# Kernel tuning notes

Hardware: AMD Instinct MI355X
Metric: run time of the kernel (lower is better)

## Reference

```python
import jax, jax.numpy as jnp
import numpy as np

# ---- model constants (match init_kwargs) ----
B, N, T, L = 16384, 32, 300, 1
DIM = 2                      # len(state_index)
DT = 1.0 / (T * L)           # dt = 1/(T*l)
STEPS = T * L                # Euler integration steps (time_steps = STEPS+1)
A_X = 1.0                    # canonical DMP phase constant
TAU = 1.0
HID = 64
OUT = N * DIM + DIM          # fc2_mean output size


def setup_inputs() -> dict:
    key = jax.random.key(0)
    ks = jax.random.split(key, 8)
    s = lambda i, shape, scale: jax.random.normal(ks[i], shape, jnp.float32) * scale
    inp = {
        "state": jax.random.normal(ks[0], (B, 3), jnp.float32),
        "fc1_w": s(1, (HID, 3), 0.3),
        "fc1_b": jnp.full((HID,), 0.1, jnp.float32),
        "fc2m_w": s(2, (OUT, HID), 0.1),
        "fc2m_b": jnp.full((OUT,), 0.1, jnp.float32),
        "sig_w": s(3, (DIM, HID), 0.1),
        "sig_b": jnp.zeros((DIM,), jnp.float32),
        "val_w": s(4, (DIM, HID), 0.1),
        "val_b": jnp.zeros((DIM,), jnp.float32),
    }
    # DMPParameters: gaussian RBF centers on exp-decayed phase, canonical widths
    c = jnp.exp(-A_X * jnp.linspace(0.0, 1.0, N))
    inp["dmp_c"] = c.astype(jnp.float32)
    inp["dmp_sigma2"] = (N ** 1.5 / c / A_X).astype(jnp.float32)
    return inp


def dmp_rollout(w, goal, y0, dy0, a_z, c, sigma2):
    """Euler rollout of DMP transformation system.
    w: [M,N] basis weights, goal/y0/dy0/a_z: [M] per-channel scalars.
    Returns Y, dY, ddY each [M, STEPS+1]."""
    z0 = dy0 * TAU
    b_z = a_z / 4.0

    def step(carry, _):
        x, y, z = carry
        x = x + (-A_X * x) * TAU * DT                       # phase update
        psi = jnp.exp(-0.5 * (x - c) ** 2 / sigma2)          # [N] gaussian RBF
        fx = (w @ psi) * x * (goal - y0) / jnp.sum(psi)      # [M] forcing term
        dz = a_z * (b_z * (goal - y) - z) + fx
        dy = z
        y = y + TAU * dy * DT
        z = z + TAU * dz * DT
        return (x, y, z), (y, dy * TAU, dz * TAU)

    _, (Ys, dYs, ddYs) = jax.lax.scan(
        step, (jnp.float32(1.0), y0, z0), None, length=STEPS)
    Y = jnp.concatenate([y0[None], Ys], axis=0).T            # [M, STEPS+1]
    dY = jnp.concatenate([dy0[None], dYs], axis=0).T
    ddY = jnp.concatenate([z0[None], ddYs], axis=0).T
    return Y, dY, ddY


def reference(state, fc1_w, fc1_b, fc2m_w, fc2m_b, sig_w, sig_b,
              val_w, val_b, dmp_c, dmp_sigma2):
    x = jnp.tanh(state @ fc1_w.T + fc1_b) * 0.1              # [B,64]
    y0 = state[:, :DIM].reshape(-1)                           # [M=B*DIM]
    dy0 = jnp.zeros_like(y0) + 0.01

    # value = fc2_value(x).repeat(1,T).view(-1,T,2).transpose(1,2) == broadcast over T
    v = x @ val_w.T + val_b                                   # [B,2]
    value = jnp.broadcast_to(v[:, :, None], (B, DIM, T))

    sigma = (jax.nn.sigmoid(x @ sig_w.T + sig_b) * 1.0 + 0.001).reshape(-1, DIM, 1)

    ndp_wg = x @ fc2m_w.T + fc2m_b                            # [B, 2N+2]
    goal = ndp_wg[:, :DIM].reshape(-1)                        # [M]
    w = ndp_wg[:, DIM:DIM * (N + 1)].reshape(-1, N)           # [M,N]
    a_z = jnp.clip(ndp_wg[:, -1], 0.5, 30.0)                  # learned a_z (az=True)
    a_z = jnp.broadcast_to(a_z[:, None], (B, DIM)).reshape(-1)

    Y, _, _ = dmp_rollout(w, goal, y0, dy0, a_z, dmp_c, dmp_sigma2)
    y = Y.reshape(B, DIM, -1)[:, :, ::L]                      # [B,2,T+1]
    a = y[:, :, 1:] - y[:, :, :-1]                            # [B,2,T]
    return (a, sigma, value)
```

## Files before the change

kernel.cpp:

```cpp
#include <hip/hip_runtime.h>
#include <hip/hip_bf16.h>

#define NB 32
#define TS 300
#define TSP 304
#define NBATCH 16384
#define DTF (1.0f/300.0f)
#define A_ELEMS (NBATCH*2*TS)

typedef __attribute__((ext_vector_type(8))) short bf16x8;
typedef __attribute__((ext_vector_type(4))) float f32x4;

static __device__ __forceinline__ ushort f2bf(float f) {
    union { __hip_bfloat16 h; ushort u; } cv;
    cv.h = __float2bfloat16(f);
    return cv.u;
}
static __device__ __forceinline__ float rdlane(float v, int lane) {
    return __int_as_float(__builtin_amdgcn_readlane(__float_as_int(v), lane));
}

__global__ __launch_bounds__(256) void k_head(
    const float* __restrict__ state,
    const float* __restrict__ fc1_w, const float* __restrict__ fc1_b,
    const float* __restrict__ fc2m_w, const float* __restrict__ fc2m_b,
    const float* __restrict__ sig_w, const float* __restrict__ sig_b,
    const float* __restrict__ val_w, const float* __restrict__ val_b,
    const float* __restrict__ dmp_c, const float* __restrict__ dmp_s2,
    float* __restrict__ sig_out, float* __restrict__ pbuf,
    ushort* __restrict__ wbuf16, ushort* __restrict__ phiB)
{
    if (blockIdx.x == 512) {
        const float l2 = log2f(1.0f - DTF);
        for (int t = threadIdx.x; t < TSP; t += 256) {
            ushort row[NB];
            if (t < TS) {
                const float x = exp2f((float)(t + 1) * l2);
                float ps[NB]; float s = 0.0f;
                #pragma unroll
                for (int n = 0; n < NB; ++n) {
                    float d = x - dmp_c[n];
                    float p = __expf(-0.5f * d * d / dmp_s2[n]);
                    ps[n] = p; s += p;
                }
                const float inv = x / s;
                #pragma unroll
                for (int n = 0; n < NB; ++n) row[n] = f2bf(ps[n] * inv);
            } else {
                #pragma unroll
                for (int n = 0; n < NB; ++n) row[n] = 0;
            }
            uint4* dst = (uint4*)(phiB + t*NB);
            #pragma unroll
            for (int q4 = 0; q4 < 4; ++q4) {
                union { ushort us[8]; uint4 v; } pk;
                #pragma unroll
                for (int e = 0; e < 8; ++e) pk.us[e] = row[q4*8 + e];
                dst[q4] = pk.v;
            }
        }
        return;
    }

    __shared__ float wlds[70*64];
    __shared__ float f1[64*4];
    const int tid = threadIdx.x;
    const int wv_ = tid >> 6;
    const int j   = tid & 63;

    for (int i = tid; i < 70*64; i += 256) {
        const int row = i >> 6, col = i & 63;
        float v;
        if (row < 66)      v = fc2m_w[i];
        else if (row < 68) v = sig_w[(row-66)*64 + col];
        else               v = val_w[(row-68)*64 + col];
        const int q = col >> 2, e = col & 3;
        wlds[row*64 + (((q ^ (row & 15)) << 2) | e)] = v;
    }
    if (tid < 64) {
        f1[tid*4+0] = fc1_w[tid*3+0];
        f1[tid*4+1] = fc1_w[tid*3+1];
        f1[tid*4+2] = fc1_w[tid*3+2];
        f1[tid*4+3] = fc1_b[tid];
    }
    __syncthreads();

    const int r2 = 64 + (j % 6);
    float wr[64], w2[64];
    #pragma unroll
    for (int q = 0; q < 16; ++q) {
        float4 a  = *(const float4*)(wlds + j*64  + ((q ^ (j  & 15)) << 2));
        wr[q*4+0]=a.x; wr[q*4+1]=a.y; wr[q*4+2]=a.z; wr[q*4+3]=a.w;
        float4 b4 = *(const float4*)(wlds + r2*64 + ((q ^ (r2 & 15)) << 2));
        w2[q*4+0]=b4.x; w2[q*4+1]=b4.y; w2[q*4+2]=b4.z; w2[q*4+3]=b4.w;
    }
    const float bias1 = fc2m_b[j];
    const float bias2 = (r2 < 66) ? fc2m_b[r2] : (r2 < 68) ? sig_b[r2-66] : val_b[r2-68];
    const float4 fw = *(const float4*)(f1 + j*4);

    const int bbase = (blockIdx.x << 5) + (wv_ << 3);
    float sreg = (j < 24) ? state[bbase*3 + j] : 0.0f;

    for (int it = 0; it < 8; ++it) {
        const int b = bbase + it;
        const float s0  = rdlane(sreg, it*3+0);
        const float s1  = rdlane(sreg, it*3+1);
        const float s2v = rdlane(sreg, it*3+2);
        float pre = fmaf(fw.x, s0, fmaf(fw.y, s1, fmaf(fw.z, s2v, fw.w)));
        float e = __expf(2.0f * pre);
        float h = (1.0f - 2.0f/(e + 1.0f)) * 0.1f;
        float a1 = bias1, a1b = 0.0f, a2 = bias2, a2b = 0.0f;
        #pragma unroll
        for (int k = 0; k < 64; k += 2) {
            const float h0 = rdlane(h, k);
            const float h1 = rdlane(h, k+1);
            a1  = fmaf(wr[k],   h0, a1 );
            a1b = fmaf(wr[k+1], h1, a1b);
            a2  = fmaf(w2[k],   h0, a2 );
            a2b = fmaf(w2[k+1], h1, a2b);
        }
        a1 += a1b; a2 += a2b;
        float az = rdlane(a2, 1);
        az = fminf(fmaxf(az, 0.5f), 30.0f);
        const float vv0 = rdlane(a2, 4);
        const float vv1 = rdlane(a2, 5);
        if (j >= 2) wbuf16[b*64 + j - 2]  = f2bf(a1);
        else        wbuf16[b*64 + 62 + j] = f2bf(a2);
        if (j == 2 || j == 3)
            sig_out[b*2 + j - 2] = 1.0f / (1.0f + __expf(-a2)) + 0.001f;
        if (j < 2) {
            const float y0 = (j == 0) ? s0 : s1;
            const float vvl = (j == 0) ? vv0 : vv1;
            *(float4*)(pbuf + (b*2 + j)*4) = make_float4(a1, a1 - y0, az, vvl);
        }
    }
}

__global__ __launch_bounds__(256) void k_rollout(
    const ushort* __restrict__ phiB, const float* __restrict__ pbuf,
    const ushort* __restrict__ wbuf16, float* __restrict__ a_out,
    float* __restrict__ v_out)
{
    __shared__ float tile[256][20];
    const int tid = threadIdx.x;
    const int wv = tid >> 6;
    const int l  = tid & 63;
    const int ch = l & 15;
    const int g  = l >> 4;
    const int m  = (blockIdx.x << 6) + (wv << 4) + ch;

    const float4 pp = *(const float4*)(pbuf + m*4);
    const float az = pp.z;
    const float Ac = DTF * az * az * 0.25f;
    const float Bc = DTF * az;
    const float Kc = DTF * pp.y;
    const float c0 = (g == 0) ? Ac * pp.x : 0.0f;
    float y = (g == 0) ? (pp.x - pp.y) : 0.0f;
    float z = (g == 0) ? 0.01f : 0.0f;

    const bf16x8 wb = *(const bf16x8*)(wbuf16 + m*NB + g*8);
    const bf16x8* ap = (const bf16x8*)(phiB + ch*NB + g*8);
    bf16x8 af = ap[0];

    const float fv = pp.w;
    const f32x4 zacc = {0.0f, 0.0f, 0.0f, 0.0f};
    float4* myrow = (float4*)&tile[tid][0];

    for (int c = 0; c < 19; ++c) {
        f32x4 facc = __builtin_amdgcn_mfma_f32_16x16x32_bf16(af, wb, zacc, 0, 0, 0);
        if (c < 18) af = ap[(c + 1) * 64];
        float av[16];
        #pragma unroll
        for (int i = 0; i < 16; ++i) {
            float f = (g == (i >> 2)) ? facc[i & 3] : 0.0f;
            av[i] = z * DTF;
            float u = z + c0;
            u = fmaf(Kc, f, u);
            u = fmaf(-Bc, z, u);
            z = fmaf(-Ac, y, u);
            y += av[i];
        }
        #pragma unroll
        for (int q = 0; q < 4; ++q)
            myrow[q] = make_float4(av[q*4+0], av[q*4+1], av[q*4+2], av[q*4+3]);

        if (c < 18 || g < 3) {
            float4 s4 = make_float4(0.f, 0.f, 0.f, 0.f);
            #pragma unroll
            for (int gg = 0; gg < 4; ++gg) {
                const float4 v4 = *(const float4*)&tile[(wv << 6) + (gg << 4) + ch][g << 2];
                s4.x += v4.x; s4.y += v4.y; s4.z += v4.z; s4.w += v4.w;
            }
            const int ob = m * TS + c*16 + (g << 2);
            *(float4*)(a_out + ob) = s4;
            *(float4*)(v_out + ob) = make_float4(fv, fv, fv, fv);
        }
    }
}

extern "C" void kernel_launch(void* const* d_in, const int* in_sizes, int n_in,
                              void* d_out, int out_size, void* d_ws, size_t ws_size,
                              hipStream_t stream) {
    (void)in_sizes; (void)n_in; (void)out_size; (void)ws_size;
    const float* state  = (const float*)d_in[0];
    const float* fc1_w  = (const float*)d_in[1];
    const float* fc1_b  = (const float*)d_in[2];
    const float* fc2m_w = (const float*)d_in[3];
    const float* fc2m_b = (const float*)d_in[4];
    const float* sig_w  = (const float*)d_in[5];
    const float* sig_b  = (const float*)d_in[6];
    const float* val_w  = (const float*)d_in[7];
    const float* val_b  = (const float*)d_in[8];
    const float* dmp_c  = (const float*)d_in[9];
    const float* dmp_s2 = (const float*)d_in[10];

    float* out     = (float*)d_out;
    float* a_out   = out;
    float* sig_out = out + A_ELEMS;
    float* v_out   = out + A_ELEMS + NBATCH*2;

    float* ws     = (float*)d_ws;
    ushort* phiB  = (ushort*)ws;
    float* pbuf   = ws + 8192;
    ushort* wbuf16 = (ushort*)(ws + 8192 + 131072);

    k_head<<<dim3(513), dim3(256), 0, stream>>>(state, fc1_w, fc1_b, fc2m_w, fc2m_b,
                                                sig_w, sig_b, val_w, val_b,
                                                dmp_c, dmp_s2,
                                                sig_out, pbuf, wbuf16, phiB);
    k_rollout<<<dim3(512), dim3(256), 0, stream>>>(phiB, pbuf, wbuf16, a_out, v_out);
}
```

Before: 33.95 us.

## Fuse head and rollout kernels, keep intermediates in LDS, broadcast forcing via permlane

```diff
diff --git a/kernel.cpp b/kernel.cpp
--- a/kernel.cpp
+++ b/kernel.cpp
@@ -3,7 +3,6 @@
 
 #define NB 32
 #define TS 300
-#define TSP 304
 #define NBATCH 16384
 #define DTF (1.0f/300.0f)
 #define A_ELEMS (NBATCH*2*TS)
@@ -20,52 +19,25 @@
     return __int_as_float(__builtin_amdgcn_readlane(__float_as_int(v), lane));
 }
 
-__global__ __launch_bounds__(256) void k_head(
+__global__ __launch_bounds__(256) void k_fused(
     const float* __restrict__ state,
     const float* __restrict__ fc1_w, const float* __restrict__ fc1_b,
     const float* __restrict__ fc2m_w, const float* __restrict__ fc2m_b,
     const float* __restrict__ sig_w, const float* __restrict__ sig_b,
     const float* __restrict__ val_w, const float* __restrict__ val_b,
     const float* __restrict__ dmp_c, const float* __restrict__ dmp_s2,
-    float* __restrict__ sig_out, float* __restrict__ pbuf,
-    ushort* __restrict__ wbuf16, ushort* __restrict__ phiB)
+    float* __restrict__ sig_out, float* __restrict__ a_out,
+    float* __restrict__ v_out)
 {
-    if (blockIdx.x == 512) {
-        const float l2 = log2f(1.0f - DTF);
-        for (int t = threadIdx.x; t < TSP; t += 256) {
-            ushort row[NB];
-            if (t < TS) {
-                const float x = exp2f((float)(t + 1) * l2);
-                float ps[NB]; float s = 0.0f;
-                #pragma unroll
-                for (int n = 0; n < NB; ++n) {
-                    float d = x - dmp_c[n];
-                    float p = __expf(-0.5f * d * d / dmp_s2[n]);
-                    ps[n] = p; s += p;
-                }
-                const float inv = x / s;
-                #pragma unroll
-                for (int n = 0; n < NB; ++n) row[n] = f2bf(ps[n] * inv);
-            } else {
-                #pragma unroll
-                for (int n = 0; n < NB; ++n) row[n] = 0;
-            }
-            uint4* dst = (uint4*)(phiB + t*NB);
-            #pragma unroll
-            for (int q4 = 0; q4 < 4; ++q4) {
-                union { ushort us[8]; uint4 v; } pk;
-                #pragma unroll
-                for (int e = 0; e < 8; ++e) pk.us[e] = row[q4*8 + e];
-                dst[q4] = pk.v;
-            }
-        }
-        return;
-    }
-
-    __shared__ float wlds[70*64];
-    __shared__ float f1[64*4];
+    __shared__ ushort phis[304*NB];
+    __shared__ float  wlds[70*64];
+    __shared__ float  f1[64*4];
+    __shared__ ushort wloc[64*NB];
+    __shared__ float4 ppl[64];
+    __shared__ float4 xt[4][16][5];
+
     const int tid = threadIdx.x;
-    const int wv_ = tid >> 6;
+    const int wv  = tid >> 6;
     const int j   = tid & 63;
 
     for (int i = tid; i < 70*64; i += 256) {
@@ -83,125 +55,159 @@
         f1[tid*4+2] = fc1_w[tid*3+2];
         f1[tid*4+3] = fc1_b[tid];
     }
+    {
+        const float l2 = log2f(1.0f - DTF);
+        for (int t = tid; t < 304; t += 256) {
+            ushort row[NB];
+            if (t < TS) {
+                const float x = exp2f((float)(t + 1) * l2);
+                float ps[NB]; float s = 0.0f;
+                #pragma unroll
+                for (int n = 0; n < NB; ++n) {
+                    float d = x - dmp_c[n];
+                    float p = __expf(-0.5f * d * d / dmp_s2[n]);
+                    ps[n] = p; s += p;
+                }
+                const float inv = x / s;
+                #pragma unroll
+                for (int n = 0; n < NB; ++n) row[n] = f2bf(ps[n] * inv);
+            } else {
+                #pragma unroll
+                for (int n = 0; n < NB; ++n) row[n] = 0;
+            }
+            uint4* dst = (uint4*)(phis + t*NB);
+            #pragma unroll
+            for (int q4 = 0; q4 < 4; ++q4) {
+                union { ushort us[8]; uint4 v; } pk;
+                #pragma unroll
+                for (int e = 0; e < 8; ++e) pk.us[e] = row[q4*8 + e];
+                dst[q4 ^ (t & 3)] = pk.v;
+            }
+        }
+    }
     __syncthreads();
 
-    const int r2 = 64 + (j % 6);
-    float wr[64], w2[64];
-    #pragma unroll
-    for (int q = 0; q < 16; ++q) {
-        float4 a  = *(const float4*)(wlds + j*64  + ((q ^ (j  & 15)) << 2));
-        wr[q*4+0]=a.x; wr[q*4+1]=a.y; wr[q*4+2]=a.z; wr[q*4+3]=a.w;
-        float4 b4 = *(const float4*)(wlds + r2*64 + ((q ^ (r2 & 15)) << 2));
-        w2[q*4+0]=b4.x; w2[q*4+1]=b4.y; w2[q*4+2]=b4.z; w2[q*4+3]=b4.w;
-    }
-    const float bias1 = fc2m_b[j];
-    const float bias2 = (r2 < 66) ? fc2m_b[r2] : (r2 < 68) ? sig_b[r2-66] : val_b[r2-68];
-    const float4 fw = *(const float4*)(f1 + j*4);
-
-    const int bbase = (blockIdx.x << 5) + (wv_ << 3);
-    float sreg = (j < 24) ? state[bbase*3 + j] : 0.0f;
-
-    for (int it = 0; it < 8; ++it) {
-        const int b = bbase + it;
-        const float s0  = rdlane(sreg, it*3+0);
-        const float s1  = rdlane(sreg, it*3+1);
-        const float s2v = rdlane(sreg, it*3+2);
-        float pre = fmaf(fw.x, s0, fmaf(fw.y, s1, fmaf(fw.z, s2v, fw.w)));
-        float e = __expf(2.0f * pre);
-        float h = (1.0f - 2.0f/(e + 1.0f)) * 0.1f;
-        float a1 = bias1, a1b = 0.0f, a2 = bias2, a2b = 0.0f;
+    {
+        const int r2 = 64 + (j % 6);
+        float wr[64], w2[64];
         #pragma unroll
-        for (int k = 0; k < 64; k += 2) {
-            const float h0 = rdlane(h, k);
-            const float h1 = rdlane(h, k+1);
-            a1  = fmaf(wr[k],   h0, a1 );
-            a1b = fmaf(wr[k+1], h1, a1b);
-            a2  = fmaf(w2[k],   h0, a2 );
-            a2b = fmaf(w2[k+1], h1, a2b);
-        }
-        a1 += a1b; a2 += a2b;
-        float az = rdlane(a2, 1);
-        az = fminf(fmaxf(az, 0.5f), 30.0f);
-        const float vv0 = rdlane(a2, 4);
-        const float vv1 = rdlane(a2, 5);
-        if (j >= 2) wbuf16[b*64 + j - 2]  = f2bf(a1);
-        else        wbuf16[b*64 + 62 + j] = f2bf(a2);
-        if (j == 2 || j == 3)
-            sig_out[b*2 + j - 2] = 1.0f / (1.0f + __expf(-a2)) + 0.001f;
-        if (j < 2) {
-            const float y0 = (j == 0) ? s0 : s1;
-            const float vvl = (j == 0) ? vv0 : vv1;
-            *(float4*)(pbuf + (b*2 + j)*4) = make_float4(a1, a1 - y0, az, vvl);
-        }
-    }
-}
-
-__global__ __launch_bounds__(256) void k_rollout(
-    const ushort* __restrict__ phiB, const float* __restrict__ pbuf,
-    const ushort* __restrict__ wbuf16, float* __restrict__ a_out,
-    float* __restrict__ v_out)
-{
-    __shared__ float tile[256][20];
-    const int tid = threadIdx.x;
-    const int wv = tid >> 6;
-    const int l  = tid & 63;
-    const int ch = l & 15;
-    const int g  = l >> 4;
-    const int m  = (blockIdx.x << 6) + (wv << 4) + ch;
-
-    const float4 pp = *(const float4*)(pbuf + m*4);
+        for (int q = 0; q < 16; ++q) {
+            float4 a  = *(const float4*)(wlds + j*64  + ((q ^ (j  & 15)) << 2));
+            wr[q*4+0]=a.x; wr[q*4+1]=a.y; wr[q*4+2]=a.z; wr[q*4+3]=a.w;
+            float4 b4 = *(const float4*)(wlds + r2*64 + ((q ^ (r2 & 15)) << 2));
+            w2[q*4+0]=b4.x; w2[q*4+1]=b4.y; w2[q*4+2]=b4.z; w2[q*4+3]=b4.w;
+        }
+        const float bias1 = fc2m_b[j];
+        const float bias2 = (r2 < 66) ? fc2m_b[r2] : (r2 < 68) ? sig_b[r2-66] : val_b[r2-68];
+        const float4 fw = *(const float4*)(f1 + j*4);
+
+        const int bbase = (blockIdx.x << 5) + (wv << 3);
+        float sreg = (j < 24) ? state[bbase*3 + j] : 0.0f;
+
+        for (int it = 0; it < 8; ++it) {
+            const float s0  = rdlane(sreg, it*3+0);
+            const float s1  = rdlane(sreg, it*3+1);
+            const float s2v = rdlane(sreg, it*3+2);
+            float pre = fmaf(fw.x, s0, fmaf(fw.y, s1, fmaf(fw.z, s2v, fw.w)));
+            float e = __expf(2.0f * pre);
+            float h = (1.0f - 2.0f/(e + 1.0f)) * 0.1f;
+            float a1 = bias1, a1b = 0.0f, a2 = bias2, a2b = 0.0f;
+            #pragma unroll
+            for (int k = 0; k < 64; k += 2) {
+                const float h0 = rdlane(h, k);
+                const float h1 = rdlane(h, k+1);
+                a1  = fmaf(wr[k],   h0, a1 );
+                a1b = fmaf(wr[k+1], h1, a1b);
+                a2  = fmaf(w2[k],   h0, a2 );
+                a2b = fmaf(w2[k+1], h1, a2b);
+            }
+            a1 += a1b; a2 += a2b;
+            float az = rdlane(a2, 1);
+            az = fminf(fmaxf(az, 0.5f), 30.0f);
+            const float vv0 = rdlane(a2, 4);
+            const float vv1 = rdlane(a2, 5);
+            const int chp = (wv << 4) + (it << 1);
+            if (j >= 2) wloc[(chp + ((j-2) >> 5))*NB + ((j-2) & 31)] = f2bf(a1);
+            else        wloc[(chp + 1)*NB + 30 + j]                  = f2bf(a2);
+            if (j == 2 || j == 3)
+                sig_out[(bbase + it)*2 + j - 2] = 1.0f / (1.0f + __expf(-a2)) + 0.001f;
+            if (j < 2) {
+                const float y0 = (j == 0) ? s0 : s1;
+                const float vvl = (j == 0) ? vv0 : vv1;
+                ppl[chp + j] = make_float4(a1, a1 - y0, az, vvl);
+            }
+        }
+    }
+    __syncthreads();
+
+    const int ch = j & 15;
+    const int g  = j >> 4;
+    const int chl = (wv << 4) + ch;
+
+    const float4 pp = ppl[chl];
     const float az = pp.z;
     const float Ac = DTF * az * az * 0.25f;
     const float Bc = DTF * az;
     const float Kc = DTF * pp.y;
-    const float c0 = (g == 0) ? Ac * pp.x : 0.0f;
-    float y = (g == 0) ? (pp.x - pp.y) : 0.0f;
-    float z = (g == 0) ? 0.01f : 0.0f;
-
-    const bf16x8 wb = *(const bf16x8*)(wbuf16 + m*NB + g*8);
-    const bf16x8* ap = (const bf16x8*)(phiB + ch*NB + g*8);
-    bf16x8 af = ap[0];
-
-    const float fv = pp.w;
+    const float c0 = Ac * pp.x;
+    float y = pp.x - pp.y;
+    float z = 0.01f;
+
+    const bf16x8 wb = *(const bf16x8*)(wloc + chl*NB + g*8);
+    const ushort* aprow = phis + ch*NB + ((g ^ (ch & 3)) << 3);
+    bf16x8 af = *(const bf16x8*)aprow;
+
+    const int mloc = j >> 2;
+    const int m_st = (blockIdx.x << 6) + (wv << 4) + mloc;
+    const float fv = ppl[(wv << 4) + mloc].w;
+    const float4 vsp = make_float4(fv, fv, fv, fv);
+    float* aptr = a_out + m_st*TS + (j & 3)*4;
+    float* vptr = v_out + m_st*TS + (j & 3)*4;
+    const bool tail_ok = (j & 3) < 3;
+
     const f32x4 zacc = {0.0f, 0.0f, 0.0f, 0.0f};
-    float4* myrow = (float4*)&tile[tid][0];
 
     for (int c = 0; c < 19; ++c) {
         f32x4 facc = __builtin_amdgcn_mfma_f32_16x16x32_bf16(af, wb, zacc, 0, 0, 0);
-        if (c < 18) af = ap[(c + 1) * 64];
-        float av[16];
+        if (c < 18) af = *(const bf16x8*)(aprow + (c + 1)*16*NB);
+
+        float F[16];
+        #pragma unroll
+        for (int q = 0; q < 4; ++q) {
+            float a = facc[q], b = facc[q];
+            asm volatile("v_permlane16_swap_b32 %0, %1" : "+v"(a), "+v"(b));
+            float a2 = a, b2 = b;
+            asm volatile("v_permlane32_swap_b32 %0, %1" : "+v"(a), "+v"(a2));
+            asm volatile("v_permlane32_swap_b32 %0, %1" : "+v"(b), "+v"(b2));
+            F[0*4+q] = a; F[1*4+q] = b; F[2*4+q] = a2; F[3*4+q] = b2;
+        }
+
+        float avq[4] = {0.f, 0.f, 0.f, 0.f};
         #pragma unroll
         for (int i = 0; i < 16; ++i) {
-            float f = (g == (i >> 2)) ? facc[i & 3] : 0.0f;
-            av[i] = z * DTF;
+            const float aval = z * DTF;
+            if (g == (i >> 2)) avq[i & 3] = aval;
             float u = z + c0;
-            u = fmaf(Kc, f, u);
+            u = fmaf(Kc, F[i], u);
             u = fmaf(-Bc, z, u);
             z = fmaf(-Ac, y, u);
-            y += av[i];
-        }
-        #pragma unroll
-        for (int q = 0; q < 4; ++q)
-            myrow[q] = make_float4(av[q*4+0], av[q*4+1], av[q*4+2], av[q*4+3]);
-
-        if (c < 18 || g < 3) {
-            float4 s4 = make_float4(0.f, 0.f, 0.f, 0.f);
-            #pragma unroll
-            for (int gg = 0; gg < 4; ++gg) {
-                const float4 v4 = *(const float4*)&tile[(wv << 6) + (gg << 4) + ch][g << 2];
-                s4.x += v4.x; s4.y += v4.y; s4.z += v4.z; s4.w += v4.w;
-            }
-            const int ob = m * TS + c*16 + (g << 2);
-            *(float4*)(a_out + ob) = s4;
-            *(float4*)(v_out + ob) = make_float4(fv, fv, fv, fv);
-        }
+            y += aval;
+        }
+
+        xt[wv][ch][g] = make_float4(avq[0], avq[1], avq[2], avq[3]);
+        if (c < 18 || tail_ok) {
+            const float4 s4 = xt[wv][mloc][j & 3];
+            *(float4*)aptr = s4;
+            *(float4*)vptr = vsp;
+        }
+        aptr += 16; vptr += 16;
     }
 }
 
 extern "C" void kernel_launch(void* const* d_in, const int* in_sizes, int n_in,
                               void* d_out, int out_size, void* d_ws, size_t ws_size,
                               hipStream_t stream) {
-    (void)in_sizes; (void)n_in; (void)out_size; (void)ws_size;
+    (void)in_sizes; (void)n_in; (void)out_size; (void)d_ws; (void)ws_size;
     const float* state  = (const float*)d_in[0];
     const float* fc1_w  = (const float*)d_in[1];
     const float* fc1_b  = (const float*)d_in[2];
@@ -219,14 +225,8 @@
     float* sig_out = out + A_ELEMS;
     float* v_out   = out + A_ELEMS + NBATCH*2;
 
-    float* ws     = (float*)d_ws;
-    ushort* phiB  = (ushort*)ws;
-    float* pbuf   = ws + 8192;
-    ushort* wbuf16 = (ushort*)(ws + 8192 + 131072);
-
-    k_head<<<dim3(513), dim3(256), 0, stream>>>(state, fc1_w, fc1_b, fc2m_w, fc2m_b,
-                                                sig_w, sig_b, val_w, val_b,
-                                                dmp_c, dmp_s2,
-                                                sig_out, pbuf, wbuf16, phiB);
-    k_rollout<<<dim3(512), dim3(256), 0, stream>>>(phiB, pbuf, wbuf16, a_out, v_out);
-}
+    k_fused<<<dim3(512), dim3(256), 0, stream>>>(state, fc1_w, fc1_b, fc2m_w, fc2m_b,
+                                                 sig_w, sig_b, val_w, val_b,
+                                                 dmp_c, dmp_s2,
+                                                 sig_out, a_out, v_out);
+}
```

Result: no change. 33.98 us (+0.1%).
